# Optimization experiments

Hardware: AMD Instinct MI355X
Metric: run time of the kernel (lower is better)

Reference implementation:

```python
import jax, jax.numpy as jnp
import numpy as np

N_NODES = 50000
N_EDGES = 800000
IN_F, HID, EMB = 10, 256, 128
BN_EPS = 1e-5


def _glorot(key, shape):
    fan_in, fan_out = shape[0], shape[1]
    lim = (6.0 / (fan_in + fan_out)) ** 0.5
    return jax.random.uniform(key, shape, jnp.float32, -lim, lim)


def setup_inputs() -> dict:
    key = jax.random.key(0)
    ks = jax.random.split(key, 16)
    inp = {
        "x": jax.random.normal(ks[0], (N_NODES, IN_F), jnp.float32),
        "edge_index": jax.random.randint(ks[1], (2, N_EDGES), 0, N_NODES, jnp.int64),
        # input_proj: Linear(10,256) + BN
        "w_in": _glorot(ks[2], (IN_F, HID)),
        "b_in": jnp.zeros((HID,), jnp.float32),
        "g_in": jnp.ones((HID,), jnp.float32),
        "be_in": jnp.zeros((HID,), jnp.float32),
        # SAGEConv 1 (256->256): lin_l (neighbor aggr, with bias), lin_r (root, no bias)
        "wl1": _glorot(ks[3], (HID, HID)), "bl1": jnp.zeros((HID,), jnp.float32), "wr1": _glorot(ks[4], (HID, HID)),
        "g1": jnp.ones((HID,), jnp.float32), "be1": jnp.zeros((HID,), jnp.float32),
        # SAGEConv 2 (256->256)
        "wl2": _glorot(ks[5], (HID, HID)), "bl2": jnp.zeros((HID,), jnp.float32), "wr2": _glorot(ks[6], (HID, HID)),
        "g2": jnp.ones((HID,), jnp.float32), "be2": jnp.zeros((HID,), jnp.float32),
        # SAGEConv 3 (256->128)
        "wl3": _glorot(ks[7], (HID, EMB)), "bl3": jnp.zeros((EMB,), jnp.float32), "wr3": _glorot(ks[8], (HID, EMB)),
    }
    return inp


def _bn(h, g, b):
    # BatchNorm1d in training-mode math (batch statistics, biased variance)
    mu = jnp.mean(h, axis=0)
    var = jnp.var(h, axis=0)
    return (h - mu) * jax.lax.rsqrt(var + BN_EPS) * g + b


def _sage(h, src, dst, wl, bl, wr):
    # mean aggregation of neighbor messages: gather h[src], scatter-mean into dst
    msg = h[src]                                             # [E, d]
    s = jax.ops.segment_sum(msg, dst, num_segments=N_NODES)  # [N, d]
    cnt = jax.ops.segment_sum(jnp.ones((msg.shape[0],), h.dtype), dst, num_segments=N_NODES)
    agg = s / jnp.maximum(cnt, 1.0)[:, None]                 # isolated nodes -> 0
    return agg @ wl + bl + h @ wr


def reference(x, edge_index, w_in, b_in, g_in, be_in,
              wl1, bl1, wr1, g1, be1,
              wl2, bl2, wr2, g2, be2,
              wl3, bl3, wr3):
    src, dst = edge_index[0], edge_index[1]
    # input_proj: Linear + BN + ReLU (dropout disabled for determinism)
    h = jax.nn.relu(_bn(x @ w_in + b_in, g_in, be_in))
    h = jax.nn.relu(_bn(_sage(h, src, dst, wl1, bl1, wr1), g1, be1))
    h = jax.nn.relu(_bn(_sage(h, src, dst, wl2, bl2, wr2), g2, be2))
    h = _sage(h, src, dst, wl3, bl3, wr3)
    return h
```

## Files before the change

kernel.cpp:

```cpp
#include <hip/hip_runtime.h>

#define N_NODES 50000
#define N_EDGES 800000
#define IN_F 10
#define HID 256
#define EMB 128
#define BN_EPS 1e-5f
#define N_SCAN_BLKS ((N_NODES + 255) / 256)
#define CNT_BLKS (N_EDGES / 256)
#define WCONV_ELEMS (4 * HID * HID + 2 * EMB * HID)
#define WCONV_BLKS (WCONV_ELEMS / 256)
#define SSTRIDE 512
#define NSHARD 8
#define NPART 8
#define PART_SZ (N_NODES / NPART)
#define SCAT_BLKS 2048

typedef __attribute__((ext_vector_type(8))) short short8;
typedef __attribute__((ext_vector_type(4))) float floatx4;
typedef __attribute__((ext_vector_type(2))) float floatx2;

__device__ __forceinline__ unsigned short f2bf(float f) {
    unsigned u = __float_as_uint(f);
    unsigned r = (u + 0x7fffu + ((u >> 16) & 1u)) >> 16;
    return (unsigned short)r;
}
__device__ __forceinline__ float bf_lo(unsigned int u) { return __uint_as_float(u << 16); }
__device__ __forceinline__ float bf_hi(unsigned int u) { return __uint_as_float(u & 0xffff0000u); }
__device__ __forceinline__ float bf2f(unsigned short s) { return __uint_as_float(((unsigned)s) << 16); }

__device__ __forceinline__ void gload_lds16(const unsigned short* g, unsigned short* l) {
    __builtin_amdgcn_global_load_lds(
        (const __attribute__((address_space(1))) unsigned int*)(uintptr_t)(const void*)g,
        (__attribute__((address_space(3))) unsigned int*)(unsigned int)(uintptr_t)(void*)l,
        16, 0, 0);
}

__global__ void k_count_wconv(const int* __restrict__ e_dst, int* __restrict__ cnt,
                              const float* __restrict__ wl1, const float* __restrict__ wr1,
                              const float* __restrict__ wl2, const float* __restrict__ wr2,
                              const float* __restrict__ wl3, const float* __restrict__ wr3,
                              unsigned short* __restrict__ wl1t, unsigned short* __restrict__ wr1t,
                              unsigned short* __restrict__ wl2t, unsigned short* __restrict__ wr2t,
                              unsigned short* __restrict__ wl3t, unsigned short* __restrict__ wr3t) {
    int b = blockIdx.x;
    int t = threadIdx.x;
    if (b < CNT_BLKS) {
        atomicAdd(&cnt[e_dst[b * 256 + t]], 1);
        return;
    }
    int idx = (b - CNT_BLKS) * 256 + t;
    const int S = HID * HID;
    if (idx < 4 * S) {
        int sel = idx >> 16;
        int o = idx & (S - 1);
        const float* w = sel == 0 ? wl1 : sel == 1 ? wr1 : sel == 2 ? wl2 : wr2;
        unsigned short* wt = sel == 0 ? wl1t : sel == 1 ? wr1t : sel == 2 ? wl2t : wr2t;
        int n = o >> 8, k = o & 255;
        wt[o] = f2bf(w[k * HID + n]);
    } else {
        int r = idx - 4 * S;
        int sel = r >> 15;
        int o = r & 32767;
        const float* w = sel ? wr3 : wl3;
        unsigned short* wt = sel ? wr3t : wl3t;
        int n = o >> 8, k = o & 255;
        wt[o] = f2bf(w[k * EMB + n]);
    }
}

__global__ void k_reduce_cnt(const int* __restrict__ cnt, int* __restrict__ part) {
    __shared__ int sdata[256];
    int i = blockIdx.x * 256 + threadIdx.x;
    sdata[threadIdx.x] = (i < N_NODES) ? cnt[i] : 0;
    __syncthreads();
    for (int off = 128; off > 0; off >>= 1) {
        if (threadIdx.x < off) sdata[threadIdx.x] += sdata[threadIdx.x + off];
        __syncthreads();
    }
    if (threadIdx.x == 0) part[blockIdx.x] = sdata[0];
}

__global__ void k_scan_part(const int* __restrict__ part, int* __restrict__ partoff,
                            int* __restrict__ row_off_last) {
    __shared__ int buf[256];
    int tid = threadIdx.x;
    int v = (tid < N_SCAN_BLKS) ? part[tid] : 0;
    buf[tid] = v;
    __syncthreads();
    for (int off = 1; off < 256; off <<= 1) {
        int t = (tid >= off) ? buf[tid - off] : 0;
        __syncthreads();
        buf[tid] += t;
        __syncthreads();
    }
    if (tid < N_SCAN_BLKS) partoff[tid] = buf[tid] - v;
    if (tid == 255) *row_off_last = buf[255];
}

__global__ void k_scan_final(const int* __restrict__ cnt, const int* __restrict__ partoff,
                             int* __restrict__ row_off, int* __restrict__ fill_pos) {
    __shared__ int buf[256];
    int tid = threadIdx.x;
    int i = blockIdx.x * 256 + tid;
    int v = (i < N_NODES) ? cnt[i] : 0;
    buf[tid] = v;
    __syncthreads();
    for (int off = 1; off < 256; off <<= 1) {
        int t = (tid >= off) ? buf[tid - off] : 0;
        __syncthreads();
        buf[tid] += t;
        __syncthreads();
    }
    if (i < N_NODES) {
        int excl = partoff[blockIdx.x] + buf[tid] - v;
        row_off[i] = excl;
        fill_pos[i] = excl;
    }
}

__global__ void k_scatter_part(const int* __restrict__ src, const int* __restrict__ dst,
                               int* __restrict__ fill_pos, int* __restrict__ sorted_src) {
    int part = blockIdx.x & 7;
    int lo = part * PART_SZ, hi = lo + PART_SZ;
    int idx = (blockIdx.x >> 3) * 256 + threadIdx.x;
    for (int e = idx; e < N_EDGES; e += (SCAT_BLKS / 8) * 256) {
        int d = dst[e];
        if (d >= lo && d < hi) {
            int p = atomicAdd(&fill_pos[d], 1);
            sorted_src[p] = src[e];
        }
    }
}

#define IP_BLOCKS 1024
__global__ __launch_bounds__(256) void k_input_proj(
        const float* __restrict__ x, const float* __restrict__ w,
        const float* __restrict__ bias, unsigned short* __restrict__ h,
        float* __restrict__ stats) {
    __shared__ float sbuf[2048];
    __shared__ float qbuf[2048];
    int t = threadIdx.x;
    int jg = t & 31;
    int ns = t >> 5;
    int j0 = jg * 8;

    float wreg[IN_F][8];
#pragma unroll
    for (int k = 0; k < IN_F; k++)
#pragma unroll
        for (int c = 0; c < 8; c++) wreg[k][c] = w[k * HID + j0 + c];
    float bj[8];
#pragma unroll
    for (int c = 0; c < 8; c++) bj[c] = bias[j0 + c];

    float s[8] = {}, q[8] = {};
    const int stride = IP_BLOCKS * 8;
    for (int base = blockIdx.x * 8 + ns; base < N_NODES; base += stride) {
        float xr[IN_F];
#pragma unroll
        for (int k = 0; k < IN_F; k++) xr[k] = x[base * IN_F + k];
        float acc[8];
#pragma unroll
        for (int c = 0; c < 8; c++) {
            float a = bj[c];
#pragma unroll
            for (int k = 0; k < IN_F; k++) a += xr[k] * wreg[k][c];
            acc[c] = a;
            s[c] += a;
            q[c] += a * a;
        }
        uint4 o;
        o.x = (unsigned)f2bf(acc[0]) | ((unsigned)f2bf(acc[1]) << 16);
        o.y = (unsigned)f2bf(acc[2]) | ((unsigned)f2bf(acc[3]) << 16);
        o.z = (unsigned)f2bf(acc[4]) | ((unsigned)f2bf(acc[5]) << 16);
        o.w = (unsigned)f2bf(acc[6]) | ((unsigned)f2bf(acc[7]) << 16);
        ((uint4*)h)[(size_t)base * 32 + jg] = o;
    }

#pragma unroll
    for (int c = 0; c < 8; c++) {
        sbuf[ns * 256 + j0 + c] = s[c];
        qbuf[ns * 256 + j0 + c] = q[c];
    }
    __syncthreads();
    float ss = 0.f, qq = 0.f;
#pragma unroll
    for (int n2 = 0; n2 < 8; n2++) {
        ss += sbuf[n2 * 256 + t];
        qq += qbuf[n2 * 256 + t];
    }
    atomicAdd(&stats[t], ss);
    atomicAdd(&stats[256 + t], qq);
}

__global__ void k_bn_apply_relu(unsigned short* __restrict__ h, const float* __restrict__ stats,
                                const float* __restrict__ g, const float* __restrict__ b,
                                unsigned char* __restrict__ h8) {
    int idx = blockIdx.x * 256 + threadIdx.x;
    if (idx >= N_NODES * 32) return;
    int q = idx & 31;
    int j0 = q * 8;
    const float invn = 1.0f / (float)N_NODES;
    float sc[8], sh[8];
#pragma unroll
    for (int k = 0; k < 8; k++) {
        float ssum = 0.f, qsum = 0.f;
#pragma unroll
        for (int s = 0; s < NSHARD; s++) {
            ssum += stats[s * SSTRIDE + j0 + k];
            qsum += stats[s * SSTRIDE + 256 + j0 + k];
        }
        float mu = ssum * invn;
        float var = qsum * invn - mu * mu;
        float scale = g[j0 + k] * rsqrtf(var + BN_EPS);
        sc[k] = scale;
        sh[k] = b[j0 + k] - mu * scale;
    }
    uint4 v = ((uint4*)h)[idx];
    float f0 = fmaxf(bf_lo(v.x) * sc[0] + sh[0], 0.f);
    float f1 = fmaxf(bf_hi(v.x) * sc[1] + sh[1], 0.f);
    float f2 = fmaxf(bf_lo(v.y) * sc[2] + sh[2], 0.f);
    float f3 = fmaxf(bf_hi(v.y) * sc[3] + sh[3], 0.f);
    float f4 = fmaxf(bf_lo(v.z) * sc[4] + sh[4], 0.f);
    float f5 = fmaxf(bf_hi(v.z) * sc[5] + sh[5], 0.f);
    float f6 = fmaxf(bf_lo(v.w) * sc[6] + sh[6], 0.f);
    float f7 = fmaxf(bf_hi(v.w) * sc[7] + sh[7], 0.f);
    uint4 o;
    o.x = (unsigned)f2bf(f0) | ((unsigned)f2bf(f1) << 16);
    o.y = (unsigned)f2bf(f2) | ((unsigned)f2bf(f3) << 16);
    o.z = (unsigned)f2bf(f4) | ((unsigned)f2bf(f5) << 16);
    o.w = (unsigned)f2bf(f6) | ((unsigned)f2bf(f7) << 16);
    ((uint4*)h)[idx] = o;
    if (h8) {
        unsigned pa = __builtin_amdgcn_cvt_pk_fp8_f32(f0, f1, 0u, false);
        pa = __builtin_amdgcn_cvt_pk_fp8_f32(f2, f3, pa, true);
        unsigned pb = __builtin_amdgcn_cvt_pk_fp8_f32(f4, f5, 0u, false);
        pb = __builtin_amdgcn_cvt_pk_fp8_f32(f6, f7, pb, true);
        uint2 o8; o8.x = pa; o8.y = pb;
        ((uint2*)h8)[idx] = o8;
    }
}

__global__ void k_aggregate_fp8(const unsigned char* __restrict__ h8,
                                const int* __restrict__ row_off, const int* __restrict__ cnt,
                                const int* __restrict__ sorted_src,
                                unsigned short* __restrict__ agg) {
    int node = (blockIdx.x * blockDim.x + threadIdx.x) >> 4;
    int lane = threadIdx.x & 15;
    if (node >= N_NODES) return;
    int beg = row_off[node];
    int d = cnt[node];
    int end = beg + d;
    const uint4* h4 = (const uint4*)h8;
    float a[16] = {};
    for (int e = beg; e < end; e++) {
        int s = sorted_src[e];
        uint4 v = h4[(size_t)s * 16 + lane];
        floatx2 p;
        p = __builtin_amdgcn_cvt_pk_f32_fp8(v.x, false); a[0] += p.x;  a[1] += p.y;
        p = __builtin_amdgcn_cvt_pk_f32_fp8(v.x, true);  a[2] += p.x;  a[3] += p.y;
        p = __builtin_amdgcn_cvt_pk_f32_fp8(v.y, false); a[4] += p.x;  a[5] += p.y;
        p = __builtin_amdgcn_cvt_pk_f32_fp8(v.y, true);  a[6] += p.x;  a[7] += p.y;
        p = __builtin_amdgcn_cvt_pk_f32_fp8(v.z, false); a[8] += p.x;  a[9] += p.y;
        p = __builtin_amdgcn_cvt_pk_f32_fp8(v.z, true);  a[10] += p.x; a[11] += p.y;
        p = __builtin_amdgcn_cvt_pk_f32_fp8(v.w, false); a[12] += p.x; a[13] += p.y;
        p = __builtin_amdgcn_cvt_pk_f32_fp8(v.w, true);  a[14] += p.x; a[15] += p.y;
    }
    float inv = 1.0f / (float)(d > 1 ? d : 1);
    uint4 o0, o1;
    o0.x = (unsigned)f2bf(a[0] * inv)  | ((unsigned)f2bf(a[1] * inv) << 16);
    o0.y = (unsigned)f2bf(a[2] * inv)  | ((unsigned)f2bf(a[3] * inv) << 16);
    o0.z = (unsigned)f2bf(a[4] * inv)  | ((unsigned)f2bf(a[5] * inv) << 16);
    o0.w = (unsigned)f2bf(a[6] * inv)  | ((unsigned)f2bf(a[7] * inv) << 16);
    o1.x = (unsigned)f2bf(a[8] * inv)  | ((unsigned)f2bf(a[9] * inv) << 16);
    o1.y = (unsigned)f2bf(a[10] * inv) | ((unsigned)f2bf(a[11] * inv) << 16);
    o1.z = (unsigned)f2bf(a[12] * inv) | ((unsigned)f2bf(a[13] * inv) << 16);
    o1.w = (unsigned)f2bf(a[14] * inv) | ((unsigned)f2bf(a[15] * inv) << 16);
    ((uint4*)agg)[(size_t)node * 32 + lane * 2] = o0;
    ((uint4*)agg)[(size_t)node * 32 + lane * 2 + 1] = o1;
}

__global__ void k_aggregate_add(const unsigned short* __restrict__ G, const int* __restrict__ row_off,
                                const int* __restrict__ cnt, const int* __restrict__ sorted_src,
                                float* __restrict__ out) {
    int node = (blockIdx.x * blockDim.x + threadIdx.x) >> 4;
    int lane = threadIdx.x & 15;
    if (node >= N_NODES) return;
    int beg = row_off[node];
    int d = cnt[node];
    int end = beg + d;
    const uint4* h4 = (const uint4*)G;
    float a0 = 0.f, a1 = 0.f, a2 = 0.f, a3 = 0.f, a4 = 0.f, a5 = 0.f, a6 = 0.f, a7 = 0.f;
    for (int e = beg; e < end; e++) {
        int s = sorted_src[e];
        uint4 v = h4[(size_t)s * 16 + lane];
        a0 += bf_lo(v.x); a1 += bf_hi(v.x);
        a2 += bf_lo(v.y); a3 += bf_hi(v.y);
        a4 += bf_lo(v.z); a5 += bf_hi(v.z);
        a6 += bf_lo(v.w); a7 += bf_hi(v.w);
    }
    float inv = 1.0f / (float)(d > 1 ? d : 1);
    float4* ob = (float4*)(out + (size_t)node * EMB + lane * 8);
    float4 p0 = ob[0], p1 = ob[1];
    p0.x += a0 * inv; p0.y += a1 * inv; p0.z += a2 * inv; p0.w += a3 * inv;
    p1.x += a4 * inv; p1.y += a5 * inv; p1.z += a6 * inv; p1.w += a7 * inv;
    ob[0] = p0; ob[1] = p1;
}

#define BK 64
#define LPAD 72

#define GEMM_BLKS 784

template <int NCOL, bool STATS>
__global__ __launch_bounds__(512, 4) void k_gemm_mfma(
        const unsigned short* __restrict__ A1, const unsigned short* __restrict__ B1t,
        const unsigned short* __restrict__ A2, const unsigned short* __restrict__ B2t,
        const float* __restrict__ bias, float* __restrict__ stats,
        unsigned short* __restrict__ Cout) {
    int b = blockIdx.x;
    int xcd = b & 7;
    int q = b >> 3;
    int cx = q & 1;
    int pr = (q >> 1) * 8 + xcd;
    int r0 = pr * 128;
    if (r0 >= N_NODES) return;
    int c0 = cx * 128;

    __shared__ __attribute__((aligned(16))) unsigned short As[2][128 * 64];
    __shared__ __attribute__((aligned(16))) unsigned short Bs[2][128 * 64];

    int t = threadIdx.x;
    int wave = t >> 6, lane = t & 63;
    int wm = wave >> 2, wn = wave & 3;
    int quad = lane >> 4, l15 = lane & 15;

    floatx4 acc[4][2];
#pragma unroll
    for (int i = 0; i < 4; i++)
#pragma unroll
        for (int j = 0; j < 2; j++) acc[i][j] = (floatx4){0.f, 0.f, 0.f, 0.f};

    auto stage = [&](int buf, const unsigned short* __restrict__ A,
                     const unsigned short* __restrict__ B, int k0) {
#pragma unroll
        for (int it = 0; it < 2; it++) {
            int p = it * 512 + t;
            int row = p >> 3, ps = p & 7;
            int ls = ps ^ (row & 7);
            int rr = r0 + row;
            if (rr >= N_NODES) rr = N_NODES - 1;
            gload_lds16(&A[(size_t)rr * HID + k0 + ls * 8], &As[buf][p * 8]);
        }
#pragma unroll
        for (int it = 0; it < 2; it++) {
            int p = it * 512 + t;
            int row = p >> 3, ps = p & 7;
            int ls = ps ^ (row & 7);
            gload_lds16(&B[(size_t)(c0 + row) * HID + k0 + ls * 8], &Bs[buf][p * 8]);
        }
    };

    stage(0, A1, B1t, 0);

    int cur = 0;
#pragma unroll
    for (int ph = 0; ph < 8; ph++) {
        if (ph < 7) {
            int np = ph + 1;
            stage(cur ^ 1, (np >= 4) ? A2 : A1, (np >= 4) ? B2t : B1t, (np & 3) * BK);
            asm volatile("s_waitcnt vmcnt(4)\n\ts_barrier" ::: "memory");
        } else {
            asm volatile("s_waitcnt vmcnt(0)\n\ts_barrier" ::: "memory");
        }
#pragma unroll
        for (int kc = 0; kc < 2; kc++) {
            short8 a[4], bfr[2];
            int ls = kc * 4 + quad;
#pragma unroll
            for (int i = 0; i < 4; i++) {
                int arow = wm * 64 + i * 16 + l15;
                int ps = ls ^ (arow & 7);
                a[i] = *(const short8*)&As[cur][arow * 64 + ps * 8];
            }
#pragma unroll
            for (int j = 0; j < 2; j++) {
                int brow = wn * 32 + j * 16 + l15;
                int ps = ls ^ (brow & 7);
                bfr[j] = *(const short8*)&Bs[cur][brow * 64 + ps * 8];
            }
#pragma unroll
            for (int i = 0; i < 4; i++)
#pragma unroll
                for (int j = 0; j < 2; j++)
                    acc[i][j] = __builtin_amdgcn_mfma_f32_16x16x32_bf16(a[i], bfr[j], acc[i][j], 0, 0, 0);
        }
        asm volatile("s_barrier" ::: "memory");
        cur ^= 1;
    }

    float bv[2];
#pragma unroll
    for (int j = 0; j < 2; j++) bv[j] = bias[c0 + wn * 32 + j * 16 + l15];

    float s_part[2] = {0.f, 0.f};
    float q_part[2] = {0.f, 0.f};

#pragma unroll
    for (int i = 0; i < 4; i++) {
#pragma unroll
        for (int r = 0; r < 4; r++) {
            int m = r0 + wm * 64 + i * 16 + quad * 4 + r;
            if (m >= N_NODES) continue;
#pragma unroll
            for (int j = 0; j < 2; j++) {
                int n = c0 + wn * 32 + j * 16 + l15;
                float v = acc[i][j][r] + bv[j];
                if (STATS) { s_part[j] += v; q_part[j] += v * v; }
                Cout[(size_t)m * NCOL + n] = f2bf(v);
            }
        }
    }

    if (STATS) {
        float* sred = (float*)As;
        __syncthreads();
        if (t < 256) sred[t] = 0.f;
        __syncthreads();
#pragma unroll
        for (int j = 0; j < 2; j++) {
            int cl = wn * 32 + j * 16 + l15;
            atomicAdd(&sred[cl], s_part[j]);
            atomicAdd(&sred[128 + cl], q_part[j]);
        }
        __syncthreads();
        if (t < 128) {
            int base = (pr & (NSHARD - 1)) * SSTRIDE;
            atomicAdd(&stats[base + c0 + t], sred[t]);
            atomicAdd(&stats[base + 256 + c0 + t], sred[128 + t]);
        }
    }
}

__global__ __launch_bounds__(512) void k_gemm_l3_dual(
        const unsigned short* __restrict__ A, const unsigned short* __restrict__ B1t,
        const unsigned short* __restrict__ B2t, const float* __restrict__ stats,
        const float* __restrict__ g, const float* __restrict__ be,
        const float* __restrict__ bl3, unsigned short* __restrict__ G,
        float* __restrict__ P) {
    __shared__ unsigned short As[128 * LPAD];
    __shared__ unsigned short B1s[128 * LPAD];
    __shared__ unsigned short B2s[128 * LPAD];
    __shared__ float scs[256], shs[256];
    int t = threadIdx.x;
    if (t < 256) {
        const float invn = 1.0f / (float)N_NODES;
        float ssum = 0.f, qsum = 0.f;
#pragma unroll
        for (int s = 0; s < NSHARD; s++) {
            ssum += stats[s * SSTRIDE + t];
            qsum += stats[s * SSTRIDE + 256 + t];
        }
        float mu = ssum * invn;
        float var = qsum * invn - mu * mu;
        float sc = g[t] * rsqrtf(var + BN_EPS);
        scs[t] = sc;
        shs[t] = be[t] - mu * sc;
    }
    __syncthreads();

    int wave = t >> 6, lane = t & 63;
    int wm = wave >> 2, wn = wave & 3;
    int quad = lane >> 4, l15 = lane & 15;
    int r0 = blockIdx.x * 128;
    int lrow = t >> 3;
    int lseg = t & 7;

    floatx4 acc1[4][2], acc2[4][2];
#pragma unroll
    for (int i = 0; i < 4; i++)
#pragma unroll
        for (int j = 0; j < 2; j++) {
            acc1[i][j] = (floatx4){0.f, 0.f, 0.f, 0.f};
            acc2[i][j] = (floatx4){0.f, 0.f, 0.f, 0.f};
        }

    for (int k0 = 0; k0 < HID; k0 += BK) {
        float sc8[8], sh8[8];
        int cb = k0 + lseg * 8;
#pragma unroll
        for (int c = 0; c < 8; c++) { sc8[c] = scs[cb + c]; sh8[c] = shs[cb + c]; }
#pragma unroll
        for (int it = 0; it < 2; it++) {
            int row = lrow + it * 64;
            int r = r0 + row;
            uint4 va;
            if (r < N_NODES) va = *(const uint4*)&A[(size_t)r * HID + cb];
            else va = (uint4){0u, 0u, 0u, 0u};
            float f0 = fmaxf(bf_lo(va.x) * sc8[0] + sh8[0], 0.f);
            float f1 = fmaxf(bf_hi(va.x) * sc8[1] + sh8[1], 0.f);
            float f2 = fmaxf(bf_lo(va.y) * sc8[2] + sh8[2], 0.f);
            float f3 = fmaxf(bf_hi(va.y) * sc8[3] + sh8[3], 0.f);
            float f4 = fmaxf(bf_lo(va.z) * sc8[4] + sh8[4], 0.f);
            float f5 = fmaxf(bf_hi(va.z) * sc8[5] + sh8[5], 0.f);
            float f6 = fmaxf(bf_lo(va.w) * sc8[6] + sh8[6], 0.f);
            float f7 = fmaxf(bf_hi(va.w) * sc8[7] + sh8[7], 0.f);
            if (r >= N_NODES) { f0=f1=f2=f3=f4=f5=f6=f7=0.f; }
            uint4 ov;
            ov.x = (unsigned)f2bf(f0) | ((unsigned)f2bf(f1) << 16);
            ov.y = (unsigned)f2bf(f2) | ((unsigned)f2bf(f3) << 16);
            ov.z = (unsigned)f2bf(f4) | ((unsigned)f2bf(f5) << 16);
            ov.w = (unsigned)f2bf(f6) | ((unsigned)f2bf(f7) << 16);
            *(uint4*)&As[row * LPAD + lseg * 8] = ov;
            *(uint4*)&B1s[row * LPAD + lseg * 8] = *(const uint4*)&B1t[(size_t)row * HID + cb];
            *(uint4*)&B2s[row * LPAD + lseg * 8] = *(const uint4*)&B2t[(size_t)row * HID + cb];
        }
        __syncthreads();
#pragma unroll
        for (int kc = 0; kc < 2; kc++) {
            short8 a[4], b1[2], b2[2];
#pragma unroll
            for (int i = 0; i < 4; i++)
                a[i] = *(const short8*)&As[(wm * 64 + i * 16 + l15) * LPAD + kc * 32 + quad * 8];
#pragma unroll
            for (int j = 0; j < 2; j++) {
                b1[j] = *(const short8*)&B1s[(wn * 32 + j * 16 + l15) * LPAD + kc * 32 + quad * 8];
                b2[j] = *(const short8*)&B2s[(wn * 32 + j * 16 + l15) * LPAD + kc * 32 + quad * 8];
            }
#pragma unroll
            for (int i = 0; i < 4; i++)
#pragma unroll
                for (int j = 0; j < 2; j++) {
                    acc1[i][j] = __builtin_amdgcn_mfma_f32_16x16x32_bf16(a[i], b1[j], acc1[i][j], 0, 0, 0);
                    acc2[i][j] = __builtin_amdgcn_mfma_f32_16x16x32_bf16(a[i], b2[j], acc2[i][j], 0, 0, 0);
                }
        }
        __syncthreads();
    }

    float bv[2];
#pragma unroll
    for (int j = 0; j < 2; j++) bv[j] = bl3[wn * 32 + j * 16 + l15];

#pragma unroll
    for (int i = 0; i < 4; i++) {
#pragma unroll
        for (int r = 0; r < 4; r++) {
            int m = r0 + wm * 64 + i * 16 + quad * 4 + r;
            if (m >= N_NODES) continue;
#pragma unroll
            for (int j = 0; j < 2; j++) {
                int n = wn * 32 + j * 16 + l15;
                G[(size_t)m * EMB + n] = f2bf(acc1[i][j][r]);
                P[(size_t)m * EMB + n] = acc2[i][j][r] + bv[j];
            }
        }
    }
}

extern "C" void kernel_launch(void* const* d_in, const int* in_sizes, int n_in,
                              void* d_out, int out_size, void* d_ws, size_t ws_size,
                              hipStream_t stream) {
    const float* x    = (const float*)d_in[0];
    const int*   ei   = (const int*)d_in[1];
    const float* w_in = (const float*)d_in[2];
    const float* b_in = (const float*)d_in[3];
    const float* g_in = (const float*)d_in[4];
    const float* be_in= (const float*)d_in[5];
    const float* wl1  = (const float*)d_in[6];
    const float* bl1  = (const float*)d_in[7];
    const float* wr1  = (const float*)d_in[8];
    const float* g1   = (const float*)d_in[9];
    const float* be1  = (const float*)d_in[10];
    const float* wl2  = (const float*)d_in[11];
    const float* bl2  = (const float*)d_in[12];
    const float* wr2  = (const float*)d_in[13];
    const float* g2   = (const float*)d_in[14];
    const float* be2  = (const float*)d_in[15];
    const float* wl3  = (const float*)d_in[16];
    const float* bl3  = (const float*)d_in[17];
    const float* wr3  = (const float*)d_in[18];
    float* out = (float*)d_out;

    char* p = (char*)d_ws;
    auto alloc = [&](size_t bytes) -> void* {
        void* r = (void*)p;
        p += (bytes + 255) & ~(size_t)255;
        return r;
    };
    int*   cnt    = (int*)alloc((size_t)N_NODES * 4);
    float* stats0 = (float*)alloc((size_t)NSHARD * SSTRIDE * 4);
    float* stats1 = (float*)alloc((size_t)NSHARD * SSTRIDE * 4);
    float* stats2 = (float*)alloc((size_t)NSHARD * SSTRIDE * 4);
    size_t zlen = (size_t)((char*)stats2 + NSHARD * SSTRIDE * 4 - (char*)cnt);

    unsigned short* bufA = (unsigned short*)alloc((size_t)N_NODES * HID * 2);
    unsigned short* bufB = (unsigned short*)alloc((size_t)N_NODES * HID * 2);
    unsigned short* bufC = (unsigned short*)alloc((size_t)N_NODES * HID * 2);
    unsigned char*  h8   = (unsigned char*)alloc((size_t)N_NODES * HID);
    unsigned short* wl1t = (unsigned short*)alloc((size_t)HID * HID * 2);
    unsigned short* wr1t = (unsigned short*)alloc((size_t)HID * HID * 2);
    unsigned short* wl2t = (unsigned short*)alloc((size_t)HID * HID * 2);
    unsigned short* wr2t = (unsigned short*)alloc((size_t)HID * HID * 2);
    unsigned short* wl3t = (unsigned short*)alloc((size_t)EMB * HID * 2);
    unsigned short* wr3t = (unsigned short*)alloc((size_t)EMB * HID * 2);
    int*   row_off    = (int*)alloc((size_t)(N_NODES + 1) * 4);
    int*   fill_pos   = (int*)alloc((size_t)N_NODES * 4);
    int*   sorted_src = (int*)alloc((size_t)N_EDGES * 4);
    int*   part       = (int*)alloc((size_t)256 * 4);
    int*   partoff    = (int*)alloc((size_t)256 * 4);

    const int* e_src = ei;
    const int* e_dst = ei + N_EDGES;

    hipMemsetAsync(cnt, 0, zlen, stream);
    k_count_wconv<<<CNT_BLKS + WCONV_BLKS, 256, 0, stream>>>(
        e_dst, cnt, wl1, wr1, wl2, wr2, wl3, wr3, wl1t, wr1t, wl2t, wr2t, wl3t, wr3t);
    k_reduce_cnt<<<N_SCAN_BLKS, 256, 0, stream>>>(cnt, part);
    k_scan_part<<<1, 256, 0, stream>>>(part, partoff, &row_off[N_NODES]);
    k_scan_final<<<N_SCAN_BLKS, 256, 0, stream>>>(cnt, partoff, row_off, fill_pos);
    k_scatter_part<<<SCAT_BLKS, 256, 0, stream>>>(e_src, e_dst, fill_pos, sorted_src);

    k_input_proj<<<IP_BLOCKS, 256, 0, stream>>>(x, w_in, b_in, bufA, stats0);
    k_bn_apply_relu<<<(N_NODES * 32 + 255) / 256, 256, 0, stream>>>(bufA, stats0, g_in, be_in, h8);

    int aggF8_blocks = (N_NODES * 16 + 255) / 256;

    k_aggregate_fp8<<<aggF8_blocks, 256, 0, stream>>>(h8, row_off, cnt, sorted_src, bufC);
    k_gemm_mfma<HID, true><<<GEMM_BLKS, 512, 0, stream>>>(bufC, wl1t, bufA, wr1t, bl1, stats1, bufB);
    k_bn_apply_relu<<<(N_NODES * 32 + 255) / 256, 256, 0, stream>>>(bufB, stats1, g1, be1, h8);

    k_aggregate_fp8<<<aggF8_blocks, 256, 0, stream>>>(h8, row_off, cnt, sorted_src, bufC);
    k_gemm_mfma<HID, true><<<GEMM_BLKS, 512, 0, stream>>>(bufC, wl2t, bufB, wr2t, bl2, stats2, bufA);

    k_gemm_l3_dual<<<(N_NODES + 127) / 128, 512, 0, stream>>>(
        bufA, wl3t, wr3t, stats2, g2, be2, bl3, bufB, out);
    k_aggregate_add<<<(N_NODES * 16 + 255) / 256, 256, 0, stream>>>(bufB, row_off, cnt, sorted_src, out);
}
```

Baseline: 487.8 us.

## Restructure layer-3 dual GEMM into column-split pipelined MFMA kernel; add setprio

New measurement: 486.1 us. About the same (-0.4%).

```diff
diff --git a/kernel.cpp b/kernel.cpp
--- a/kernel.cpp
+++ b/kernel.cpp
@@ -309,7 +309,6 @@
 }
 
 #define BK 64
-#define LPAD 72
 
 #define GEMM_BLKS 784
 
@@ -390,11 +389,13 @@
                 int ps = ls ^ (brow & 7);
                 bfr[j] = *(const short8*)&Bs[cur][brow * 64 + ps * 8];
             }
+            __builtin_amdgcn_s_setprio(1);
 #pragma unroll
             for (int i = 0; i < 4; i++)
 #pragma unroll
                 for (int j = 0; j < 2; j++)
                     acc[i][j] = __builtin_amdgcn_mfma_f32_16x16x32_bf16(a[i], bfr[j], acc[i][j], 0, 0, 0);
+            __builtin_amdgcn_s_setprio(0);
         }
         asm volatile("s_barrier" ::: "memory");
         cur ^= 1;
@@ -443,16 +444,27 @@
     }
 }
 
-__global__ __launch_bounds__(512) void k_gemm_l3_dual(
-        const unsigned short* __restrict__ A, const unsigned short* __restrict__ B1t,
-        const unsigned short* __restrict__ B2t, const float* __restrict__ stats,
+#define L3_BLKS 784
+
+__global__ __launch_bounds__(512, 4) void k_gemm_l3_dual(
+        const unsigned short* __restrict__ A, const unsigned short* __restrict__ Bt,
+        const float* __restrict__ stats,
         const float* __restrict__ g, const float* __restrict__ be,
         const float* __restrict__ bl3, unsigned short* __restrict__ G,
         float* __restrict__ P) {
-    __shared__ unsigned short As[128 * LPAD];
-    __shared__ unsigned short B1s[128 * LPAD];
-    __shared__ unsigned short B2s[128 * LPAD];
+    int b = blockIdx.x;
+    int xcd = b & 7;
+    int q = b >> 3;
+    int cx = q & 1;
+    int pr = (q >> 1) * 8 + xcd;
+    int r0 = pr * 128;
+    if (r0 >= N_NODES) return;
+    int c0 = cx * 128;
+
+    __shared__ __attribute__((aligned(16))) unsigned short As[128 * 64];
+    __shared__ __attribute__((aligned(16))) unsigned short Bs[2][128 * 64];
     __shared__ float scs[256], shs[256];
+
     int t = threadIdx.x;
     if (t < 256) {
         const float invn = 1.0f / (float)N_NODES;
@@ -473,70 +485,90 @@
     int wave = t >> 6, lane = t & 63;
     int wm = wave >> 2, wn = wave & 3;
     int quad = lane >> 4, l15 = lane & 15;
-    int r0 = blockIdx.x * 128;
-    int lrow = t >> 3;
-    int lseg = t & 7;
-
-    floatx4 acc1[4][2], acc2[4][2];
+
+    floatx4 acc[4][2];
 #pragma unroll
     for (int i = 0; i < 4; i++)
 #pragma unroll
-        for (int j = 0; j < 2; j++) {
-            acc1[i][j] = (floatx4){0.f, 0.f, 0.f, 0.f};
-            acc2[i][j] = (floatx4){0.f, 0.f, 0.f, 0.f};
-        }
-
-    for (int k0 = 0; k0 < HID; k0 += BK) {
-        float sc8[8], sh8[8];
-        int cb = k0 + lseg * 8;
-#pragma unroll
-        for (int c = 0; c < 8; c++) { sc8[c] = scs[cb + c]; sh8[c] = shs[cb + c]; }
-#pragma unroll
-        for (int it = 0; it < 2; it++) {
-            int row = lrow + it * 64;
-            int r = r0 + row;
-            uint4 va;
-            if (r < N_NODES) va = *(const uint4*)&A[(size_t)r * HID + cb];
-            else va = (uint4){0u, 0u, 0u, 0u};
-            float f0 = fmaxf(bf_lo(va.x) * sc8[0] + sh8[0], 0.f);
-            float f1 = fmaxf(bf_hi(va.x) * sc8[1] + sh8[1], 0.f);
-            float f2 = fmaxf(bf_lo(va.y) * sc8[2] + sh8[2], 0.f);
-            float f3 = fmaxf(bf_hi(va.y) * sc8[3] + sh8[3], 0.f);
-            float f4 = fmaxf(bf_lo(va.z) * sc8[4] + sh8[4], 0.f);
-            float f5 = fmaxf(bf_hi(va.z) * sc8[5] + sh8[5], 0.f);
-            float f6 = fmaxf(bf_lo(va.w) * sc8[6] + sh8[6], 0.f);
-            float f7 = fmaxf(bf_hi(va.w) * sc8[7] + sh8[7], 0.f);
-            if (r >= N_NODES) { f0=f1=f2=f3=f4=f5=f6=f7=0.f; }
-            uint4 ov;
-            ov.x = (unsigned)f2bf(f0) | ((unsigned)f2bf(f1) << 16);
-            ov.y = (unsigned)f2bf(f2) | ((unsigned)f2bf(f3) << 16);
-            ov.z = (unsigned)f2bf(f4) | ((unsigned)f2bf(f5) << 16);
-            ov.w = (unsigned)f2bf(f6) | ((unsigned)f2bf(f7) << 16);
-            *(uint4*)&As[row * LPAD + lseg * 8] = ov;
-            *(uint4*)&B1s[row * LPAD + lseg * 8] = *(const uint4*)&B1t[(size_t)row * HID + cb];
-            *(uint4*)&B2s[row * LPAD + lseg * 8] = *(const uint4*)&B2t[(size_t)row * HID + cb];
-        }
-        __syncthreads();
+        for (int j = 0; j < 2; j++) acc[i][j] = (floatx4){0.f, 0.f, 0.f, 0.f};
+
+    int p0_ = t, p1_ = 512 + t;
+    int row0 = p0_ >> 3, ps0 = p0_ & 7, ls0 = ps0 ^ (row0 & 7);
+    int row1 = p1_ >> 3, ps1 = p1_ & 7, ls1 = ps1 ^ (row1 & 7);
+    int ar0 = r0 + row0; if (ar0 >= N_NODES) ar0 = N_NODES - 1;
+    int ar1 = r0 + row1; if (ar1 >= N_NODES) ar1 = N_NODES - 1;
+
+    auto stageB = [&](int buf, int k0) {
+        gload_lds16(&Bt[(size_t)(c0 + row0) * HID + k0 + ls0 * 8], &Bs[buf][p0_ * 8]);
+        gload_lds16(&Bt[(size_t)(c0 + row1) * HID + k0 + ls1 * 8], &Bs[buf][p1_ * 8]);
+    };
+    auto issueA = [&](int k0, uint4& v0, uint4& v1) {
+        v0 = *(const uint4*)&A[(size_t)ar0 * HID + k0 + ls0 * 8];
+        v1 = *(const uint4*)&A[(size_t)ar1 * HID + k0 + ls1 * 8];
+    };
+    auto xform = [&](uint4 vv, int cb) -> uint4 {
+        float4 s0 = *(float4*)&scs[cb], s1 = *(float4*)&scs[cb + 4];
+        float4 h0 = *(float4*)&shs[cb], h1 = *(float4*)&shs[cb + 4];
+        float f0 = fmaxf(bf_lo(vv.x) * s0.x + h0.x, 0.f);
+        float f1 = fmaxf(bf_hi(vv.x) * s0.y + h0.y, 0.f);
+        float f2 = fmaxf(bf_lo(vv.y) * s0.z + h0.z, 0.f);
+        float f3 = fmaxf(bf_hi(vv.y) * s0.w + h0.w, 0.f);
+        float f4 = fmaxf(bf_lo(vv.z) * s1.x + h1.x, 0.f);
+        float f5 = fmaxf(bf_hi(vv.z) * s1.y + h1.y, 0.f);
+        float f6 = fmaxf(bf_lo(vv.w) * s1.z + h1.z, 0.f);
+        float f7 = fmaxf(bf_hi(vv.w) * s1.w + h1.w, 0.f);
+        uint4 ov;
+        ov.x = (unsigned)f2bf(f0) | ((unsigned)f2bf(f1) << 16);
+        ov.y = (unsigned)f2bf(f2) | ((unsigned)f2bf(f3) << 16);
+        ov.z = (unsigned)f2bf(f4) | ((unsigned)f2bf(f5) << 16);
+        ov.w = (unsigned)f2bf(f6) | ((unsigned)f2bf(f7) << 16);
+        return ov;
+    };
+
+    uint4 va0, va1, vb0, vb1;
+    stageB(0, 0);
+    issueA(0, va0, va1);
+
+    int cur = 0;
+#pragma unroll
+    for (int ph = 0; ph < 4; ph++) {
+        if (ph < 3) {
+            stageB(cur ^ 1, (ph + 1) * BK);
+            asm volatile("s_waitcnt vmcnt(2)" ::: "memory");
+        } else {
+            asm volatile("s_waitcnt vmcnt(0)" ::: "memory");
+        }
+        *(uint4*)&As[p0_ * 8] = xform(va0, ph * BK + ls0 * 8);
+        *(uint4*)&As[p1_ * 8] = xform(va1, ph * BK + ls1 * 8);
+        asm volatile("s_waitcnt lgkmcnt(0)\n\ts_barrier" ::: "memory");
+        if (ph < 3) issueA((ph + 1) * BK, vb0, vb1);
 #pragma unroll
         for (int kc = 0; kc < 2; kc++) {
-            short8 a[4], b1[2], b2[2];
+            short8 a[4], bfr[2];
+            int ls = kc * 4 + quad;
+#pragma unroll
+            for (int i = 0; i < 4; i++) {
+                int arow = wm * 64 + i * 16 + l15;
+                int ps = ls ^ (arow & 7);
+                a[i] = *(const short8*)&As[arow * 64 + ps * 8];
+            }
+#pragma unroll
+            for (int j = 0; j < 2; j++) {
+                int brow = wn * 32 + j * 16 + l15;
+                int ps = ls ^ (brow & 7);
+                bfr[j] = *(const short8*)&Bs[cur][brow * 64 + ps * 8];
+            }
+            __builtin_amdgcn_s_setprio(1);
 #pragma unroll
             for (int i = 0; i < 4; i++)
-                a[i] = *(const short8*)&As[(wm * 64 + i * 16 + l15) * LPAD + kc * 32 + quad * 8];
-#pragma unroll
-            for (int j = 0; j < 2; j++) {
-                b1[j] = *(const short8*)&B1s[(wn * 32 + j * 16 + l15) * LPAD + kc * 32 + quad * 8];
-                b2[j] = *(const short8*)&B2s[(wn * 32 + j * 16 + l15) * LPAD + kc * 32 + quad * 8];
-            }
-#pragma unroll
-            for (int i = 0; i < 4; i++)
-#pragma unroll
-                for (int j = 0; j < 2; j++) {
-                    acc1[i][j] = __builtin_amdgcn_mfma_f32_16x16x32_bf16(a[i], b1[j], acc1[i][j], 0, 0, 0);
-                    acc2[i][j] = __builtin_amdgcn_mfma_f32_16x16x32_bf16(a[i], b2[j], acc2[i][j], 0, 0, 0);
-                }
-        }
-        __syncthreads();
+#pragma unroll
+                for (int j = 0; j < 2; j++)
+                    acc[i][j] = __builtin_amdgcn_mfma_f32_16x16x32_bf16(a[i], bfr[j], acc[i][j], 0, 0, 0);
+            __builtin_amdgcn_s_setprio(0);
+        }
+        asm volatile("s_barrier" ::: "memory");
+        cur ^= 1;
+        va0 = vb0; va1 = vb1;
     }
 
     float bv[2];
@@ -552,8 +584,8 @@
 #pragma unroll
             for (int j = 0; j < 2; j++) {
                 int n = wn * 32 + j * 16 + l15;
-                G[(size_t)m * EMB + n] = f2bf(acc1[i][j][r]);
-                P[(size_t)m * EMB + n] = acc2[i][j][r] + bv[j];
+                if (cx == 0) G[(size_t)m * EMB + n] = f2bf(acc[i][j][r]);
+                else         P[(size_t)m * EMB + n] = acc[i][j][r] + bv[j];
             }
         }
     }
@@ -610,6 +642,7 @@
     int*   sorted_src = (int*)alloc((size_t)N_EDGES * 4);
     int*   part       = (int*)alloc((size_t)256 * 4);
     int*   partoff    = (int*)alloc((size_t)256 * 4);
+    (void)wr3t;
 
     const int* e_src = ei;
     const int* e_dst = ei + N_EDGES;
@@ -634,7 +667,7 @@
     k_aggregate_fp8<<<aggF8_blocks, 256, 0, stream>>>(h8, row_off, cnt, sorted_src, bufC);
     k_gemm_mfma<HID, true><<<GEMM_BLKS, 512, 0, stream>>>(bufC, wl2t, bufB, wr2t, bl2, stats2, bufA);
 
-    k_gemm_l3_dual<<<(N_NODES + 127) / 128, 512, 0, stream>>>(
-        bufA, wl3t, wr3t, stats2, g2, be2, bl3, bufB, out);
+    k_gemm_l3_dual<<<L3_BLKS, 512, 0, stream>>>(
+        bufA, wl3t, stats2, g2, be2, bl3, bufB, out);
     k_aggregate_add<<<(N_NODES * 16 + 255) / 256, 256, 0, stream>>>(bufB, row_off, cnt, sorted_src, out);
 }
```
